# Kernel optimization log

Hardware: AMD Instinct MI355X
Metric: run time of the kernel (lower is better)

Reference implementation:

```python
import jax, jax.numpy as jnp
import numpy as np

CUTOFF = 5.0

def cubic_cutoff(d):
    # f(0)=1, f(y)=0, smooth first derivatives at both ends
    y = CUTOFF
    xc = 1.0 - 1.5 * (d * d) / (y * y) + 0.5 * (d * d * d) / (y * y * y)
    return jnp.where(d <= 0.0, 1.0, jnp.where(d >= y, 0.0, xc))


def setup_inputs() -> dict:
    key = jax.random.key(0)
    ks = jax.random.split(key, 16)
    B, N, H = 64, 64, 128
    h = jax.random.normal(ks[0], (B, N, H), jnp.float32)
    x = jax.random.uniform(ks[1], (B, N, 3), jnp.float32) * 10.0  # 10A box -> partial neighbor sparsity
    node_mask = jnp.ones((B, N), dtype=bool)
    h0 = jax.random.normal(ks[2], (B, N, H), jnp.float32)
    s = lambda fin: 1.0 / np.sqrt(fin)
    # edge_mlp: Linear(2H+1 -> H), SiLU, Linear(H -> H), SiLU
    We1 = jax.random.normal(ks[3], (2 * H + 1, H), jnp.float32) * s(2 * H + 1)
    be1 = jnp.zeros((H,), jnp.float32)
    We2 = jax.random.normal(ks[4], (H, H), jnp.float32) * s(H)
    be2 = jnp.zeros((H,), jnp.float32)
    # node_mlp: Linear(H + residual_nf + H = 3H -> H), SiLU, Linear(H -> H)
    Wn1 = jax.random.normal(ks[5], (3 * H, H), jnp.float32) * s(3 * H)
    bn1 = jnp.zeros((H,), jnp.float32)
    Wn2 = jax.random.normal(ks[6], (H, H), jnp.float32) * s(H)
    bn2 = jnp.zeros((H,), jnp.float32)
    # coord_mlp: Linear(H -> H), SiLU, Linear(H -> 1, no bias, xavier gain=0.001)
    Wc1 = jax.random.normal(ks[7], (H, H), jnp.float32) * s(H)
    bc1 = jnp.zeros((H,), jnp.float32)
    Wc2 = jax.random.normal(ks[8], (H, 1), jnp.float32) * (0.001 * s(H))
    return {"h": h, "x": x, "node_mask": node_mask, "h0": h0,
            "We1": We1, "be1": be1, "We2": We2, "be2": be2,
            "Wn1": Wn1, "bn1": bn1, "Wn2": Wn2, "bn2": bn2,
            "Wc1": Wc1, "bc1": bc1, "Wc2": Wc2}


def reference(h, x, node_mask, h0, We1, be1, We2, be2, Wn1, bn1, Wn2, bn2, Wc1, bc1, Wc2):
    B, N, H = h.shape
    # pairwise distances; distances are detached in the torch default path
    diff = x[:, :, None, :] - x[:, None, :, :]                     # [B,N,N,3]
    d = jax.lax.stop_gradient(jnp.sqrt(jnp.sum(diff * diff, -1)))  # [B,N,N]
    eye = jnp.eye(N, dtype=bool)[None]
    mask = (node_mask[:, :, None] & node_mask[:, None, :]
            & (d < CUTOFF) & (~eye))                               # [B,N,N]
    maskf = mask.astype(h.dtype)
    # edge model: feat[b,j,k] = [h[b,j], h[b,k], d^2]
    feat = jnp.concatenate([
        jnp.broadcast_to(h[:, :, None, :], (B, N, N, H)),
        jnp.broadcast_to(h[:, None, :, :], (B, N, N, H)),
        (d * d)[..., None]], axis=-1)                              # [B,N,N,2H+1]
    e = jax.nn.silu(feat @ We1 + be1)
    e = jax.nn.silu(e @ We2 + be2)
    mij = e * (cubic_cutoff(d) * maskf)[..., None]                 # [B,N,N,H]
    # node model: sum messages into receiver j
    mi = jnp.sum(mij, axis=2)                                      # [B,N,H]
    nfeat = jnp.concatenate([h, mi, h0], axis=-1)                  # [B,N,3H]
    h_out = jax.nn.silu(nfeat @ Wn1 + bn1) @ Wn2 + bn2
    h_new = h + h_out                                              # recurrent
    # coord model (scatter-add semantics of the intended math)
    phi = jax.nn.silu(mij @ Wc1 + bc1) @ Wc2                       # [B,N,N,1]
    C = 1.0 / (N - 1.0)
    x_up = C * jnp.sum(diff * phi * maskf[..., None], axis=2)      # [B,N,3]
    x_new = jnp.clip(x + x_up, -1000.0, 1000.0)
    return (h_new, x_new)
```

## Files before the change

### kernel.cpp

```cpp
#include <hip/hip_runtime.h>

#define Hh 128
#define Nn 64
#define CAP 2048
#define TPB 16

typedef _Float16 f16x8 __attribute__((ext_vector_type(8)));
typedef float f32x4 __attribute__((ext_vector_type(4)));
typedef unsigned int u32;

__device__ __forceinline__ float silu_f(float v){
    return v * __builtin_amdgcn_rcpf(1.0f + __expf(-v));
}
__device__ __forceinline__ int swz(int row, int cb){ return row*256 + (cb ^ ((row & 7) << 4)); }

#define WT_BYTES (9*32768)

__global__ __launch_bounds__(128) void k_w(
    const float* __restrict__ We1, const float* __restrict__ We2, const float* __restrict__ Wc1,
    const float* __restrict__ Wn1, const float* __restrict__ Wn2, char* __restrict__ wT)
{
    if (blockIdx.x == 128){
        if (threadIdx.x < 16){
            f16x8 v;
            #pragma unroll
            for (int i=0;i<8;i++) v[i] = (_Float16)We1[256*Hh + threadIdx.x*8 + i];
            *(f16x8*)(wT + 8*32768 + threadIdx.x*16) = v;
        }
        return;
    }
    const int id  = blockIdx.x*128 + threadIdx.x;
    const int mat = id >> 11;
    const int r   = id & 2047;
    const int n   = r >> 4;
    const int kg  = r & 15;
    const float* __restrict__ src;
    int koff = 0;
    switch (mat){
        case 0: src = We2; break;
        case 1: src = Wc1; break;
        case 2: src = Wn1; break;
        case 3: src = Wn1; koff = 128; break;
        case 4: src = Wn1; koff = 256; break;
        case 5: src = Wn2; break;
        case 6: src = We1; break;
        default: src = We1; koff = 128; break;
    }
    f16x8 v;
    #pragma unroll
    for (int i=0;i<8;i++) v[i] = (_Float16)src[(koff + kg*8 + i)*Hh + n];
    *(f16x8*)(wT + mat*32768 + n*256 + kg*16) = v;
}

__global__ __launch_bounds__(256, 2) void k_preG(
    const float* __restrict__ h, const char* __restrict__ wT, const float* __restrict__ be1,
    _Float16* __restrict__ Aout, _Float16* __restrict__ Bout)
{
    __shared__ __align__(16) char sA[4096];

    const int r0  = blockIdx.x * 16;
    const int tid = threadIdx.x;
    const int w   = tid >> 6;
    const int l   = tid & 63;
    const int lrow= l & 15;
    const int lk  = l >> 4;
    const int n0 = 2*w, n1 = n0 + 1;
    const int colA = n0*16 + lrow, colB = n1*16 + lrow;

    {
        const int row = tid >> 4;
        const int g   = tid & 15;
        const float4* src = (const float4*)(h + (r0+row)*Hh + g*8);
        const float4 v0 = src[0], v1 = src[1];
        f16x8 e;
        e[0]=(_Float16)v0.x; e[1]=(_Float16)v0.y; e[2]=(_Float16)v0.z; e[3]=(_Float16)v0.w;
        e[4]=(_Float16)v1.x; e[5]=(_Float16)v1.y; e[6]=(_Float16)v1.z; e[7]=(_Float16)v1.w;
        *(f16x8*)(sA + swz(row, g*16)) = e;
    }
    __syncthreads();

    const char* WaT = wT + 6*32768;
    const char* WbT = wT + 7*32768;

    f32x4 accA[2], accB[2];
    {
        const float ba = be1[colA], bb = be1[colB];
        accA[0] = (f32x4){ba,ba,ba,ba};
        accA[1] = (f32x4){bb,bb,bb,bb};
        accB[0] = (f32x4){0.f,0.f,0.f,0.f};
        accB[1] = (f32x4){0.f,0.f,0.f,0.f};
    }
    #pragma unroll
    for (int kb=0;kb<4;kb++){
        const int cb = kb*64 + lk*16;
        const f16x8 a   = *(const f16x8*)(sA  + swz(lrow, cb));
        const f16x8 bA0 = *(const f16x8*)(WaT + (n0*16+lrow)*256 + cb);
        const f16x8 bA1 = *(const f16x8*)(WaT + (n1*16+lrow)*256 + cb);
        const f16x8 bB0 = *(const f16x8*)(WbT + (n0*16+lrow)*256 + cb);
        const f16x8 bB1 = *(const f16x8*)(WbT + (n1*16+lrow)*256 + cb);
        accA[0] = __builtin_amdgcn_mfma_f32_16x16x32_f16(a, bA0, accA[0], 0, 0, 0);
        accA[1] = __builtin_amdgcn_mfma_f32_16x16x32_f16(a, bA1, accA[1], 0, 0, 0);
        accB[0] = __builtin_amdgcn_mfma_f32_16x16x32_f16(a, bB0, accB[0], 0, 0, 0);
        accB[1] = __builtin_amdgcn_mfma_f32_16x16x32_f16(a, bB1, accB[1], 0, 0, 0);
    }
    #pragma unroll
    for (int r=0;r<4;r++){
        const int row = r0 + lk*4 + r;
        Aout[row*Hh + colA] = (_Float16)accA[0][r];
        Aout[row*Hh + colB] = (_Float16)accA[1][r];
        Bout[row*Hh + colA] = (_Float16)accB[0][r];
        Bout[row*Hh + colB] = (_Float16)accB[1][r];
    }
}

__global__ __launch_bounds__(256) void k_prep(
    const float* __restrict__ x,
    u32* __restrict__ cntB, u32* __restrict__ off_g, u32* __restrict__ cnt_g,
    u32* __restrict__ code_g, float* __restrict__ d2_g, float* __restrict__ cut_g)
{
    __shared__ float sX[192];
    __shared__ int sCnt[64], sOff[64];
    const int b   = blockIdx.x;
    const int tid = threadIdx.x;
    const int wd  = tid >> 6;
    const int l   = tid & 63;

    if (tid < 192) sX[tid] = x[b*192 + tid];
    __syncthreads();

    for (int jj = 0; jj < 16; jj++){
        const int j = wd*16 + jj;
        const float dx0 = sX[j*3+0]-sX[l*3+0];
        const float dx1 = sX[j*3+1]-sX[l*3+1];
        const float dx2 = sX[j*3+2]-sX[l*3+2];
        const float d2 = dx0*dx0 + dx1*dx1 + dx2*dx2;
        const bool valid = (l != j) && (d2 < 25.0f);
        const unsigned long long bal = __ballot(valid);
        if (l == 0) sCnt[j] = (int)__popcll(bal);
    }
    __syncthreads();
    if (tid < 64){
        int v = sCnt[tid];
        int incl = v;
        #pragma unroll
        for (int off=1; off<64; off<<=1){
            int o = __shfl_up(incl, off);
            if (l >= off) incl += o;
        }
        sOff[tid] = incl - v;
    }
    __syncthreads();
    if (tid < 64){
        off_g[b*64 + tid] = (u32)sOff[tid];
        cnt_g[b*64 + tid] = (u32)sCnt[tid];
        if (tid == 63){
            int tot = sOff[63] + sCnt[63];
            cntB[b] = (u32)(tot > CAP ? CAP : tot);
        }
    }
    for (int jj = 0; jj < 16; jj++){
        const int j = wd*16 + jj;
        const float dx0 = sX[j*3+0]-sX[l*3+0];
        const float dx1 = sX[j*3+1]-sX[l*3+1];
        const float dx2 = sX[j*3+2]-sX[l*3+2];
        const float d2 = dx0*dx0 + dx1*dx1 + dx2*dx2;
        const bool valid = (l != j) && (d2 < 25.0f);
        const unsigned long long bal = __ballot(valid);
        const int pos = __popcll(bal & ((1ull << l) - 1ull));
        if (valid){
            const int dst = sOff[j] + pos;
            if (dst < CAP){
                const int e = b*CAP + dst;
                code_g[e] = (u32)((j << 6) | l);
                d2_g[e]   = d2;
                cut_g[e]  = 1.0f - 0.06f*d2 + 0.004f*d2*sqrtf(d2);
            }
        }
    }
}

__global__ __launch_bounds__(256, 2) void k_edge(
    const _Float16* __restrict__ Ain, const _Float16* __restrict__ Bin,
    const char* __restrict__ wT,
    const float* __restrict__ be2_g, const float* __restrict__ bc1_g, const float* __restrict__ Wc2,
    const u32* __restrict__ cntB, const u32* __restrict__ code_g,
    const float* __restrict__ d2_g, const float* __restrict__ cut_g,
    float* __restrict__ mi_p, float* __restrict__ phi_g)
{
    __shared__ __align__(16) char sEM[32768];
    __shared__ int   sBj[128];
    __shared__ u32   sCode[128];
    __shared__ float sD2[128], sCut[128];
    __shared__ float sPhP[4][128];

    const int bid = blockIdx.x;
    const int b   = bid & 63;
    const int t   = bid >> 6;
    const int E_b = (int)cntB[b];
    const int r0  = t*128;
    if (r0 >= E_b) return;
    const int R   = (E_b - r0 < 128) ? (E_b - r0) : 128;
    const int MT  = (R + 15) >> 4;

    const int tid = threadIdx.x;
    const int w   = tid >> 6;
    const int l   = tid & 63;
    const int lrow= l & 15;
    const int lk  = l >> 4;
    const int n0 = 2*w, n1 = n0 + 1;
    const int colA = n0*16 + lrow, colB = n1*16 + lrow;
    const char* We2T = wT;
    const char* Wc1T = wT + 32768;

    if (tid < 128){
        if (tid < R){
            const u32 c = code_g[b*CAP + r0 + tid];
            sCode[tid] = c;
            sBj[tid]   = (int)(c >> 6);
            sD2[tid]   = d2_g[b*CAP + r0 + tid];
            sCut[tid]  = cut_g[b*CAP + r0 + tid];
        } else {
            sCode[tid] = 0; sBj[tid] = -1; sD2[tid] = 0.f; sCut[tid] = 0.f;
        }
    }
    __syncthreads();

    {
        const f16x8* W6 = (const f16x8*)(wT + 8*32768);
        #pragma unroll
        for (int pass=0; pass<2; pass++){
            const int row = pass*64 + (tid >> 2);
            if (row < MT*16){
                const int q = tid & 3;
                const u32 c = sCode[row];
                const int jl = (int)(c >> 6), kl = (int)(c & 63);
                const _Float16 d2h = (_Float16)sD2[row];
                f16x8 dsplat;
                #pragma unroll
                for (int i=0;i<8;i++) dsplat[i] = d2h;
                const f16x8* Aj = (const f16x8*)(Ain + (b*Nn+jl)*Hh + q*32);
                const f16x8* Bk = (const f16x8*)(Bin + (b*Nn+kl)*Hh + q*32);
                #pragma unroll
                for (int s=0;s<4;s++){
                    f16x8 pre = Aj[s] + Bk[s] + W6[q*4+s]*dsplat;
                    f16x8 e;
                    #pragma unroll
                    for (int i=0;i<8;i++) e[i] = (_Float16)silu_f((float)pre[i]);
                    *(f16x8*)(sEM + swz(row, q*64 + s*16)) = e;
                }
            }
        }
    }
    __syncthreads();

    f32x4 acc[4][2];
    for (int tb = 0; tb < MT; tb += 4){
        const int MTp = (MT - tb < 4) ? (MT - tb) : 4;
        {
            const float b2a = be2_g[colA], b2b = be2_g[colB];
            #pragma unroll
            for (int mt=0;mt<4;mt++){
                acc[mt][0] = (f32x4){b2a,b2a,b2a,b2a};
                acc[mt][1] = (f32x4){b2b,b2b,b2b,b2b};
            }
        }
        #pragma unroll
        for (int kb=0;kb<4;kb++){
            const int cb = kb*64 + lk*16;
            const f16x8 bA = *(const f16x8*)(We2T + (n0*16+lrow)*256 + cb);
            const f16x8 bB = *(const f16x8*)(We2T + (n1*16+lrow)*256 + cb);
            #pragma unroll
            for (int mt=0;mt<4;mt++){
                if (mt < MTp){
                    const f16x8 a = *(const f16x8*)(sEM + swz((tb+mt)*16 + lrow, cb));
                    acc[mt][0] = __builtin_amdgcn_mfma_f32_16x16x32_f16(a, bA, acc[mt][0], 0, 0, 0);
                    acc[mt][1] = __builtin_amdgcn_mfma_f32_16x16x32_f16(a, bB, acc[mt][1], 0, 0, 0);
                }
            }
        }
        #pragma unroll
        for (int mt=0;mt<4;mt++){
            if (mt < MTp){
                #pragma unroll
                for (int r=0;r<4;r++){
                    const int row = (tb+mt)*16 + lk*4 + r;
                    const float m0 = silu_f(acc[mt][0][r]) * sCut[row];
                    const float m1 = silu_f(acc[mt][1][r]) * sCut[row];
                    acc[mt][0][r] = m0; acc[mt][1][r] = m1;
                }
            }
        }
        __syncthreads();
        #pragma unroll
        for (int mt=0;mt<4;mt++){
            if (mt < MTp){
                #pragma unroll
                for (int r=0;r<4;r++){
                    const int row = (tb+mt)*16 + lk*4 + r;
                    const int xr  = (row & 7) << 4;
                    *(_Float16*)(sEM + row*256 + ((colA*2) ^ xr)) = (_Float16)acc[mt][0][r];
                    *(_Float16*)(sEM + row*256 + ((colB*2) ^ xr)) = (_Float16)acc[mt][1][r];
                }
            }
        }
    }
    __syncthreads();

    {
        const int col  = tid & 127;
        const int half = tid >> 7;
        const int slot = (t & 1)*2 + half;
        float sum = 0.f;
        int cur = -1;
        const int rbeg = half*64, rend = rbeg + 64;
        for (int r = rbeg; r < rend; ++r){
            const int bj = sBj[r];
            const float m = (float)(*(const _Float16*)(sEM + r*256 + ((col*2) ^ ((r&7)<<4))));
            if (bj != cur){
                if (cur >= 0) mi_p[((size_t)slot*4096 + (b<<6) + cur)*128 + col] = sum;
                cur = bj; sum = 0.f;
            }
            sum += m;
        }
        if (cur >= 0) mi_p[((size_t)slot*4096 + (b<<6) + cur)*128 + col] = sum;
    }

    for (int tb = 0; tb < MT; tb += 4){
        const int MTp = (MT - tb < 4) ? (MT - tb) : 4;
        {
            const float c1a = bc1_g[colA], c1b = bc1_g[colB];
            #pragma unroll
            for (int mt=0;mt<4;mt++){
                acc[mt][0] = (f32x4){c1a,c1a,c1a,c1a};
                acc[mt][1] = (f32x4){c1b,c1b,c1b,c1b};
            }
        }
        #pragma unroll
        for (int kb=0;kb<4;kb++){
            const int cb = kb*64 + lk*16;
            const f16x8 bA = *(const f16x8*)(Wc1T + (n0*16+lrow)*256 + cb);
            const f16x8 bB = *(const f16x8*)(Wc1T + (n1*16+lrow)*256 + cb);
            #pragma unroll
            for (int mt=0;mt<4;mt++){
                if (mt < MTp){
                    const f16x8 a = *(const f16x8*)(sEM + swz((tb+mt)*16 + lrow, cb));
                    acc[mt][0] = __builtin_amdgcn_mfma_f32_16x16x32_f16(a, bA, acc[mt][0], 0, 0, 0);
                    acc[mt][1] = __builtin_amdgcn_mfma_f32_16x16x32_f16(a, bB, acc[mt][1], 0, 0, 0);
                }
            }
        }
        const float wca = Wc2[colA], wcb = Wc2[colB];
        float php[16];
        #pragma unroll
        for (int mt=0;mt<4;mt++){
            if (mt < MTp){
                #pragma unroll
                for (int r=0;r<4;r++)
                    php[mt*4+r] = silu_f(acc[mt][0][r])*wca + silu_f(acc[mt][1][r])*wcb;
            }
        }
        #pragma unroll
        for (int i=0;i<16;i++){
            if ((i>>2) < MTp){
                php[i] += __shfl_xor(php[i], 1);
                php[i] += __shfl_xor(php[i], 2);
                php[i] += __shfl_xor(php[i], 4);
                php[i] += __shfl_xor(php[i], 8);
            }
        }
        if (lrow == 0){
            #pragma unroll
            for (int mt=0;mt<4;mt++){
                if (mt < MTp){
                    #pragma unroll
                    for (int r=0;r<4;r++)
                        sPhP[w][(tb+mt)*16 + lk*4 + r] = php[mt*4+r];
                }
            }
        }
    }
    __syncthreads();

    if (tid < 128 && tid < R){
        const float phi = sPhP[0][tid] + sPhP[1][tid] + sPhP[2][tid] + sPhP[3][tid];
        phi_g[b*CAP + r0 + tid] = phi;
    }
}

__global__ __launch_bounds__(256) void k_reduce(
    const float* __restrict__ x,
    const u32* __restrict__ off_g, const u32* __restrict__ cnt_g,
    const u32* __restrict__ code_g, const float* __restrict__ phi_g,
    const float* __restrict__ mi_p,
    _Float16* __restrict__ mi_g, float* __restrict__ out_x)
{
    const int tid = threadIdx.x;
    const int wd  = tid >> 6;
    const int l   = tid & 63;
    const int gid = blockIdx.x*4 + wd;
    const int b   = gid >> 6;

    #pragma unroll
    for (int p=0;p<2;p++){
        const int col = l*2 + p;
        const size_t base = (size_t)gid*128 + col;
        const float s = mi_p[base] + mi_p[(size_t)4096*128 + base]
                      + mi_p[(size_t)2*4096*128 + base] + mi_p[(size_t)3*4096*128 + base];
        mi_g[gid*Hh + col] = (_Float16)s;
    }

    const int cnt = (int)cnt_g[gid];
    const int off = (int)off_g[gid];
    float v0=0.f, v1=0.f, v2=0.f;
    if (l < cnt && (off + l) < CAP){
        const int e = b*CAP + off + l;
        const int kl = (int)(code_g[e] & 63);
        const float phi = phi_g[e];
        v0 = (x[gid*3+0] - x[(b*Nn+kl)*3+0]) * phi;
        v1 = (x[gid*3+1] - x[(b*Nn+kl)*3+1]) * phi;
        v2 = (x[gid*3+2] - x[(b*Nn+kl)*3+2]) * phi;
    }
    #pragma unroll
    for (int off2=1; off2<64; off2<<=1){
        v0 += __shfl_xor(v0, off2);
        v1 += __shfl_xor(v1, off2);
        v2 += __shfl_xor(v2, off2);
    }
    if (l == 0){
        const float C = 1.0f/63.0f;
        out_x[gid*3+0] = fminf(fmaxf(x[gid*3+0] + C*v0, -1000.f), 1000.f);
        out_x[gid*3+1] = fminf(fmaxf(x[gid*3+1] + C*v1, -1000.f), 1000.f);
        out_x[gid*3+2] = fminf(fmaxf(x[gid*3+2] + C*v2, -1000.f), 1000.f);
    }
}

__global__ __launch_bounds__(256, 2) void k_node(
    const float* __restrict__ h, const _Float16* __restrict__ mi_g,
    const float* __restrict__ h0,
    const char* __restrict__ wT,
    const float* __restrict__ bn1_g, const float* __restrict__ bn2_g,
    float* __restrict__ out_h)
{
    __shared__ __align__(16) char sA[8192];
    __shared__ __align__(16) char sHid[8192];

    const int r0  = blockIdx.x * 32;
    const int tid = threadIdx.x;
    const int w   = tid >> 6;
    const int l   = tid & 63;
    const int lrow= l & 15;
    const int lk  = l >> 4;
    const int n0 = 2*w, n1 = n0 + 1;
    const int colA = n0*16 + lrow, colB = n1*16 + lrow;

    f32x4 acc[2][2];
    {
        const float b1a = bn1_g[colA], b1b = bn1_g[colB];
        acc[0][0] = (f32x4){b1a,b1a,b1a,b1a};
        acc[0][1] = (f32x4){b1b,b1b,b1b,b1b};
        acc[1][0] = (f32x4){b1a,b1a,b1a,b1a};
        acc[1][1] = (f32x4){b1b,b1b,b1b,b1b};
    }

    const int arow = tid >> 3;
    const int g    = tid & 7;

    for (int c = 0; c < 3; c++){
        if (c == 1){
            const f16x8* src = (const f16x8*)(mi_g + (r0+arow)*Hh + g*16);
            *(f16x8*)(sA + swz(arow, g*32))      = src[0];
            *(f16x8*)(sA + swz(arow, g*32+16))   = src[1];
        } else {
            const float* base = (c == 0) ? h : h0;
            const float4* src = (const float4*)(base + (r0+arow)*Hh + g*16);
            const float4 v0=src[0], v1=src[1], v2=src[2], v3=src[3];
            f16x8 e0, e1;
            e0[0]=(_Float16)v0.x; e0[1]=(_Float16)v0.y; e0[2]=(_Float16)v0.z; e0[3]=(_Float16)v0.w;
            e0[4]=(_Float16)v1.x; e0[5]=(_Float16)v1.y; e0[6]=(_Float16)v1.z; e0[7]=(_Float16)v1.w;
            e1[0]=(_Float16)v2.x; e1[1]=(_Float16)v2.y; e1[2]=(_Float16)v2.z; e1[3]=(_Float16)v2.w;
            e1[4]=(_Float16)v3.x; e1[5]=(_Float16)v3.y; e1[6]=(_Float16)v3.z; e1[7]=(_Float16)v3.w;
            *(f16x8*)(sA + swz(arow, g*32))    = e0;
            *(f16x8*)(sA + swz(arow, g*32+16)) = e1;
        }
        __syncthreads();
        const char* Wimg = wT + (2+c)*32768;
        #pragma unroll
        for (int kb=0;kb<4;kb++){
            const int cb = kb*64 + lk*16;
            const f16x8 bA = *(const f16x8*)(Wimg + (n0*16+lrow)*256 + cb);
            const f16x8 bB = *(const f16x8*)(Wimg + (n1*16+lrow)*256 + cb);
            #pragma unroll
            for (int mt=0;mt<2;mt++){
                const f16x8 a = *(const f16x8*)(sA + swz(mt*16 + lrow, cb));
                acc[mt][0] = __builtin_amdgcn_mfma_f32_16x16x32_f16(a, bA, acc[mt][0], 0, 0, 0);
                acc[mt][1] = __builtin_amdgcn_mfma_f32_16x16x32_f16(a, bB, acc[mt][1], 0, 0, 0);
            }
        }
        __syncthreads();
    }

    #pragma unroll
    for (int mt=0;mt<2;mt++){
        #pragma unroll
        for (int r=0;r<4;r++){
            const int row = mt*16 + lk*4 + r;
            const int xr  = (row & 7) << 4;
            *(_Float16*)(sHid + row*256 + ((colA*2) ^ xr)) = (_Float16)silu_f(acc[mt][0][r]);
            *(_Float16*)(sHid + row*256 + ((colB*2) ^ xr)) = (_Float16)silu_f(acc[mt][1][r]);
        }
    }
    __syncthreads();

    const char* Wn2T = wT + 5*32768;
    f32x4 acc2[2][2];
    {
        const float b2a = bn2_g[colA], b2b = bn2_g[colB];
        acc2[0][0] = (f32x4){b2a,b2a,b2a,b2a};
        acc2[0][1] = (f32x4){b2b,b2b,b2b,b2b};
        acc2[1][0] = (f32x4){b2a,b2a,b2a,b2a};
        acc2[1][1] = (f32x4){b2b,b2b,b2b,b2b};
    }
    #pragma unroll
    for (int kb=0;kb<4;kb++){
        const int cb = kb*64 + lk*16;
        const f16x8 bA = *(const f16x8*)(Wn2T + (n0*16+lrow)*256 + cb);
        const f16x8 bB = *(const f16x8*)(Wn2T + (n1*16+lrow)*256 + cb);
        #pragma unroll
        for (int mt=0;mt<2;mt++){
            const f16x8 a = *(const f16x8*)(sHid + swz(mt*16 + lrow, cb));
            acc2[mt][0] = __builtin_amdgcn_mfma_f32_16x16x32_f16(a, bA, acc2[mt][0], 0, 0, 0);
            acc2[mt][1] = __builtin_amdgcn_mfma_f32_16x16x32_f16(a, bB, acc2[mt][1], 0, 0, 0);
        }
    }
    #pragma unroll
    for (int mt=0;mt<2;mt++){
        #pragma unroll
        for (int r=0;r<4;r++){
            const int row = r0 + mt*16 + lk*4 + r;
            out_h[row*Hh + colA] = h[row*Hh + colA] + acc2[mt][0][r];
            out_h[row*Hh + colB] = h[row*Hh + colB] + acc2[mt][1][r];
        }
    }
}

extern "C" void kernel_launch(void* const* d_in, const int* in_sizes, int n_in,
                              void* d_out, int out_size, void* d_ws, size_t ws_size,
                              hipStream_t stream) {
    const float* h   = (const float*)d_in[0];
    const float* x   = (const float*)d_in[1];
    const float* h0  = (const float*)d_in[3];
    const float* We1 = (const float*)d_in[4];
    const float* be1 = (const float*)d_in[5];
    const float* We2 = (const float*)d_in[6];
    const float* be2 = (const float*)d_in[7];
    const float* Wn1 = (const float*)d_in[8];
    const float* bn1 = (const float*)d_in[9];
    const float* Wn2 = (const float*)d_in[10];
    const float* bn2 = (const float*)d_in[11];
    const float* Wc1 = (const float*)d_in[12];
    const float* bc1 = (const float*)d_in[13];
    const float* Wc2 = (const float*)d_in[14];

    float* out_h = (float*)d_out;
    float* out_x = out_h + 64*64*128;

    char*      wT   = (char*)d_ws;
    _Float16*  A    = (_Float16*)(wT + WT_BYTES);
    _Float16*  Bv   = A + 4096*128;
    _Float16*  mi   = Bv + 4096*128;
    u32*       cntB = (u32*)(mi + 4096*128);
    u32*       offg = cntB + 64;
    u32*       cntg = offg + 4096;
    u32*       code = cntg + 4096;
    float*     d2g  = (float*)(code + 64*CAP);
    float*     cutg = d2g + 64*CAP;
    float*     phig = cutg + 64*CAP;
    float*     mip  = phig + 64*CAP;

    hipMemsetAsync(mip, 0, (size_t)4*4096*128*sizeof(float), stream);
    k_w     <<<129, 128, 0, stream>>>(We1, We2, Wc1, Wn1, Wn2, wT);
    k_preG  <<<256, 256, 0, stream>>>(h, wT, be1, A, Bv);
    k_prep  <<<64, 256, 0, stream>>>(x, cntB, offg, cntg, code, d2g, cutg);
    k_edge  <<<64*TPB, 256, 0, stream>>>(A, Bv, wT, be2, bc1, Wc2,
                                         cntB, code, d2g, cutg, mip, phig);
    k_reduce<<<1024, 256, 0, stream>>>(x, offg, cntg, code, phig, mip, mi, out_x);
    k_node  <<<128, 256, 0, stream>>>(h, mi, h0, wT, bn1, bn2, out_h);
}
```

Before: 93.04 us.

## Fuse weight prep with neighbor prep, split edge LDS, drop partial-sum memset

Merges the weight-transpose kernel and the neighbor-list prep kernel into one launch, with blocks 0-63 building the edge lists and the rest converting weights. The edge kernel now keeps the first hidden layer and the masked messages in separate LDS buffers, so the coord MLP runs before the message segment-sum and one barrier goes away. The memset of the partial message buffer is removed, and the reduce kernel works out from offsets which partial slots each node wrote and reads only those. This cuts a launch, a memset and some global reads, but doubles the edge kernel's LDS to 64KB, which may lower occupancy.

```diff
diff --git a/kernel.cpp b/kernel.cpp
--- a/kernel.cpp
+++ b/kernel.cpp
@@ -16,114 +16,53 @@
 
 #define WT_BYTES (9*32768)
 
-__global__ __launch_bounds__(128) void k_w(
+__global__ __launch_bounds__(256) void k_wp(
+    const float* __restrict__ x,
     const float* __restrict__ We1, const float* __restrict__ We2, const float* __restrict__ Wc1,
-    const float* __restrict__ Wn1, const float* __restrict__ Wn2, char* __restrict__ wT)
-{
-    if (blockIdx.x == 128){
-        if (threadIdx.x < 16){
-            f16x8 v;
-            #pragma unroll
-            for (int i=0;i<8;i++) v[i] = (_Float16)We1[256*Hh + threadIdx.x*8 + i];
-            *(f16x8*)(wT + 8*32768 + threadIdx.x*16) = v;
-        }
-        return;
-    }
-    const int id  = blockIdx.x*128 + threadIdx.x;
-    const int mat = id >> 11;
-    const int r   = id & 2047;
-    const int n   = r >> 4;
-    const int kg  = r & 15;
-    const float* __restrict__ src;
-    int koff = 0;
-    switch (mat){
-        case 0: src = We2; break;
-        case 1: src = Wc1; break;
-        case 2: src = Wn1; break;
-        case 3: src = Wn1; koff = 128; break;
-        case 4: src = Wn1; koff = 256; break;
-        case 5: src = Wn2; break;
-        case 6: src = We1; break;
-        default: src = We1; koff = 128; break;
-    }
-    f16x8 v;
-    #pragma unroll
-    for (int i=0;i<8;i++) v[i] = (_Float16)src[(koff + kg*8 + i)*Hh + n];
-    *(f16x8*)(wT + mat*32768 + n*256 + kg*16) = v;
-}
-
-__global__ __launch_bounds__(256, 2) void k_preG(
-    const float* __restrict__ h, const char* __restrict__ wT, const float* __restrict__ be1,
-    _Float16* __restrict__ Aout, _Float16* __restrict__ Bout)
-{
-    __shared__ __align__(16) char sA[4096];
-
-    const int r0  = blockIdx.x * 16;
-    const int tid = threadIdx.x;
-    const int w   = tid >> 6;
-    const int l   = tid & 63;
-    const int lrow= l & 15;
-    const int lk  = l >> 4;
-    const int n0 = 2*w, n1 = n0 + 1;
-    const int colA = n0*16 + lrow, colB = n1*16 + lrow;
-
-    {
-        const int row = tid >> 4;
-        const int g   = tid & 15;
-        const float4* src = (const float4*)(h + (r0+row)*Hh + g*8);
-        const float4 v0 = src[0], v1 = src[1];
-        f16x8 e;
-        e[0]=(_Float16)v0.x; e[1]=(_Float16)v0.y; e[2]=(_Float16)v0.z; e[3]=(_Float16)v0.w;
-        e[4]=(_Float16)v1.x; e[5]=(_Float16)v1.y; e[6]=(_Float16)v1.z; e[7]=(_Float16)v1.w;
-        *(f16x8*)(sA + swz(row, g*16)) = e;
-    }
-    __syncthreads();
-
-    const char* WaT = wT + 6*32768;
-    const char* WbT = wT + 7*32768;
-
-    f32x4 accA[2], accB[2];
-    {
-        const float ba = be1[colA], bb = be1[colB];
-        accA[0] = (f32x4){ba,ba,ba,ba};
-        accA[1] = (f32x4){bb,bb,bb,bb};
-        accB[0] = (f32x4){0.f,0.f,0.f,0.f};
-        accB[1] = (f32x4){0.f,0.f,0.f,0.f};
-    }
-    #pragma unroll
-    for (int kb=0;kb<4;kb++){
-        const int cb = kb*64 + lk*16;
-        const f16x8 a   = *(const f16x8*)(sA  + swz(lrow, cb));
-        const f16x8 bA0 = *(const f16x8*)(WaT + (n0*16+lrow)*256 + cb);
-        const f16x8 bA1 = *(const f16x8*)(WaT + (n1*16+lrow)*256 + cb);
-        const f16x8 bB0 = *(const f16x8*)(WbT + (n0*16+lrow)*256 + cb);
-        const f16x8 bB1 = *(const f16x8*)(WbT + (n1*16+lrow)*256 + cb);
-        accA[0] = __builtin_amdgcn_mfma_f32_16x16x32_f16(a, bA0, accA[0], 0, 0, 0);
-        accA[1] = __builtin_amdgcn_mfma_f32_16x16x32_f16(a, bA1, accA[1], 0, 0, 0);
-        accB[0] = __builtin_amdgcn_mfma_f32_16x16x32_f16(a, bB0, accB[0], 0, 0, 0);
-        accB[1] = __builtin_amdgcn_mfma_f32_16x16x32_f16(a, bB1, accB[1], 0, 0, 0);
-    }
-    #pragma unroll
-    for (int r=0;r<4;r++){
-        const int row = r0 + lk*4 + r;
-        Aout[row*Hh + colA] = (_Float16)accA[0][r];
-        Aout[row*Hh + colB] = (_Float16)accA[1][r];
-        Bout[row*Hh + colA] = (_Float16)accB[0][r];
-        Bout[row*Hh + colB] = (_Float16)accB[1][r];
-    }
-}
-
-__global__ __launch_bounds__(256) void k_prep(
-    const float* __restrict__ x,
+    const float* __restrict__ Wn1, const float* __restrict__ Wn2, char* __restrict__ wT,
     u32* __restrict__ cntB, u32* __restrict__ off_g, u32* __restrict__ cnt_g,
     u32* __restrict__ code_g, float* __restrict__ d2_g, float* __restrict__ cut_g)
 {
+    const int tid = threadIdx.x;
+    if (blockIdx.x >= 64){
+        if (blockIdx.x == 128){
+            if (tid < 16){
+                f16x8 v;
+                #pragma unroll
+                for (int i=0;i<8;i++) v[i] = (_Float16)We1[256*Hh + tid*8 + i];
+                *(f16x8*)(wT + 8*32768 + tid*16) = v;
+            }
+            return;
+        }
+        const int id  = (blockIdx.x-64)*256 + tid;
+        const int mat = id >> 11;
+        const int r   = id & 2047;
+        const int n   = r >> 4;
+        const int kg  = r & 15;
+        const float* __restrict__ src;
+        int koff = 0;
+        switch (mat){
+            case 0: src = We2; break;
+            case 1: src = Wc1; break;
+            case 2: src = Wn1; break;
+            case 3: src = Wn1; koff = 128; break;
+            case 4: src = Wn1; koff = 256; break;
+            case 5: src = Wn2; break;
+            case 6: src = We1; break;
+            default: src = We1; koff = 128; break;
+        }
+        f16x8 v;
+        #pragma unroll
+        for (int i=0;i<8;i++) v[i] = (_Float16)src[(koff + kg*8 + i)*Hh + n];
+        *(f16x8*)(wT + mat*32768 + n*256 + kg*16) = v;
+        return;
+    }
+
     __shared__ float sX[192];
     __shared__ int sCnt[64], sOff[64];
-    const int b   = blockIdx.x;
-    const int tid = threadIdx.x;
-    const int wd  = tid >> 6;
-    const int l   = tid & 63;
+    const int b  = blockIdx.x;
+    const int wd = tid >> 6;
+    const int l  = tid & 63;
 
     if (tid < 192) sX[tid] = x[b*192 + tid];
     __syncthreads();
@@ -179,6 +118,67 @@
     }
 }
 
+__global__ __launch_bounds__(256, 2) void k_preG(
+    const float* __restrict__ h, const char* __restrict__ wT, const float* __restrict__ be1,
+    _Float16* __restrict__ Aout, _Float16* __restrict__ Bout)
+{
+    __shared__ __align__(16) char sA[4096];
+
+    const int r0  = blockIdx.x * 16;
+    const int tid = threadIdx.x;
+    const int w   = tid >> 6;
+    const int l   = tid & 63;
+    const int lrow= l & 15;
+    const int lk  = l >> 4;
+    const int n0 = 2*w, n1 = n0 + 1;
+    const int colA = n0*16 + lrow, colB = n1*16 + lrow;
+
+    {
+        const int row = tid >> 4;
+        const int g   = tid & 15;
+        const float4* src = (const float4*)(h + (r0+row)*Hh + g*8);
+        const float4 v0 = src[0], v1 = src[1];
+        f16x8 e;
+        e[0]=(_Float16)v0.x; e[1]=(_Float16)v0.y; e[2]=(_Float16)v0.z; e[3]=(_Float16)v0.w;
+        e[4]=(_Float16)v1.x; e[5]=(_Float16)v1.y; e[6]=(_Float16)v1.z; e[7]=(_Float16)v1.w;
+        *(f16x8*)(sA + swz(row, g*16)) = e;
+    }
+    __syncthreads();
+
+    const char* WaT = wT + 6*32768;
+    const char* WbT = wT + 7*32768;
+
+    f32x4 accA[2], accB[2];
+    {
+        const float ba = be1[colA], bb = be1[colB];
+        accA[0] = (f32x4){ba,ba,ba,ba};
+        accA[1] = (f32x4){bb,bb,bb,bb};
+        accB[0] = (f32x4){0.f,0.f,0.f,0.f};
+        accB[1] = (f32x4){0.f,0.f,0.f,0.f};
+    }
+    #pragma unroll
+    for (int kb=0;kb<4;kb++){
+        const int cb = kb*64 + lk*16;
+        const f16x8 a   = *(const f16x8*)(sA  + swz(lrow, cb));
+        const f16x8 bA0 = *(const f16x8*)(WaT + (n0*16+lrow)*256 + cb);
+        const f16x8 bA1 = *(const f16x8*)(WaT + (n1*16+lrow)*256 + cb);
+        const f16x8 bB0 = *(const f16x8*)(WbT + (n0*16+lrow)*256 + cb);
+        const f16x8 bB1 = *(const f16x8*)(WbT + (n1*16+lrow)*256 + cb);
+        accA[0] = __builtin_amdgcn_mfma_f32_16x16x32_f16(a, bA0, accA[0], 0, 0, 0);
+        accA[1] = __builtin_amdgcn_mfma_f32_16x16x32_f16(a, bA1, accA[1], 0, 0, 0);
+        accB[0] = __builtin_amdgcn_mfma_f32_16x16x32_f16(a, bB0, accB[0], 0, 0, 0);
+        accB[1] = __builtin_amdgcn_mfma_f32_16x16x32_f16(a, bB1, accB[1], 0, 0, 0);
+    }
+    #pragma unroll
+    for (int r=0;r<4;r++){
+        const int row = r0 + lk*4 + r;
+        Aout[row*Hh + colA] = (_Float16)accA[0][r];
+        Aout[row*Hh + colB] = (_Float16)accA[1][r];
+        Bout[row*Hh + colA] = (_Float16)accB[0][r];
+        Bout[row*Hh + colB] = (_Float16)accB[1][r];
+    }
+}
+
 __global__ __launch_bounds__(256, 2) void k_edge(
     const _Float16* __restrict__ Ain, const _Float16* __restrict__ Bin,
     const char* __restrict__ wT,
@@ -187,7 +187,8 @@
     const float* __restrict__ d2_g, const float* __restrict__ cut_g,
     float* __restrict__ mi_p, float* __restrict__ phi_g)
 {
-    __shared__ __align__(16) char sEM[32768];
+    __shared__ __align__(16) char sE1[32768];
+    __shared__ __align__(16) char sM[32768];
     __shared__ int   sBj[128];
     __shared__ u32   sCode[128];
     __shared__ float sD2[128], sCut[128];
@@ -246,7 +247,7 @@
                     f16x8 e;
                     #pragma unroll
                     for (int i=0;i<8;i++) e[i] = (_Float16)silu_f((float)pre[i]);
-                    *(f16x8*)(sEM + swz(row, q*64 + s*16)) = e;
+                    *(f16x8*)(sE1 + swz(row, q*64 + s*16)) = e;
                 }
             }
         }
@@ -272,7 +273,7 @@
             #pragma unroll
             for (int mt=0;mt<4;mt++){
                 if (mt < MTp){
-                    const f16x8 a = *(const f16x8*)(sEM + swz((tb+mt)*16 + lrow, cb));
+                    const f16x8 a = *(const f16x8*)(sE1 + swz((tb+mt)*16 + lrow, cb));
                     acc[mt][0] = __builtin_amdgcn_mfma_f32_16x16x32_f16(a, bA, acc[mt][0], 0, 0, 0);
                     acc[mt][1] = __builtin_amdgcn_mfma_f32_16x16x32_f16(a, bB, acc[mt][1], 0, 0, 0);
                 }
@@ -286,25 +287,69 @@
                     const int row = (tb+mt)*16 + lk*4 + r;
                     const float m0 = silu_f(acc[mt][0][r]) * sCut[row];
                     const float m1 = silu_f(acc[mt][1][r]) * sCut[row];
-                    acc[mt][0][r] = m0; acc[mt][1][r] = m1;
+                    const int xr  = (row & 7) << 4;
+                    *(_Float16*)(sM + row*256 + ((colA*2) ^ xr)) = (_Float16)m0;
+                    *(_Float16*)(sM + row*256 + ((colB*2) ^ xr)) = (_Float16)m1;
                 }
             }
         }
-        __syncthreads();
+    }
+    __syncthreads();
+
+    for (int tb = 0; tb < MT; tb += 4){
+        const int MTp = (MT - tb < 4) ? (MT - tb) : 4;
+        {
+            const float c1a = bc1_g[colA], c1b = bc1_g[colB];
+            #pragma unroll
+            for (int mt=0;mt<4;mt++){
+                acc[mt][0] = (f32x4){c1a,c1a,c1a,c1a};
+                acc[mt][1] = (f32x4){c1b,c1b,c1b,c1b};
+            }
+        }
+        #pragma unroll
+        for (int kb=0;kb<4;kb++){
+            const int cb = kb*64 + lk*16;
+            const f16x8 bA = *(const f16x8*)(Wc1T + (n0*16+lrow)*256 + cb);
+            const f16x8 bB = *(const f16x8*)(Wc1T + (n1*16+lrow)*256 + cb);
+            #pragma unroll
+            for (int mt=0;mt<4;mt++){
+                if (mt < MTp){
+                    const f16x8 a = *(const f16x8*)(sM + swz((tb+mt)*16 + lrow, cb));
+                    acc[mt][0] = __builtin_amdgcn_mfma_f32_16x16x32_f16(a, bA, acc[mt][0], 0, 0, 0);
+                    acc[mt][1] = __builtin_amdgcn_mfma_f32_16x16x32_f16(a, bB, acc[mt][1], 0, 0, 0);
+                }
+            }
+        }
+        const float wca = Wc2[colA], wcb = Wc2[colB];
+        float php[16];
         #pragma unroll
         for (int mt=0;mt<4;mt++){
             if (mt < MTp){
                 #pragma unroll
-                for (int r=0;r<4;r++){
-                    const int row = (tb+mt)*16 + lk*4 + r;
-                    const int xr  = (row & 7) << 4;
-                    *(_Float16*)(sEM + row*256 + ((colA*2) ^ xr)) = (_Float16)acc[mt][0][r];
-                    *(_Float16*)(sEM + row*256 + ((colB*2) ^ xr)) = (_Float16)acc[mt][1][r];
+                for (int r=0;r<4;r++)
+                    php[mt*4+r] = silu_f(acc[mt][0][r])*wca + silu_f(acc[mt][1][r])*wcb;
+            }
+        }
+        #pragma unroll
+        for (int i=0;i<16;i++){
+            if ((i>>2) < MTp){
+                php[i] += __shfl_xor(php[i], 1);
+                php[i] += __shfl_xor(php[i], 2);
+                php[i] += __shfl_xor(php[i], 4);
+                php[i] += __shfl_xor(php[i], 8);
+            }
+        }
+        if (lrow == 0){
+            #pragma unroll
+            for (int mt=0;mt<4;mt++){
+                if (mt < MTp){
+                    #pragma unroll
+                    for (int r=0;r<4;r++)
+                        sPhP[w][(tb+mt)*16 + lk*4 + r] = php[mt*4+r];
                 }
             }
         }
     }
-    __syncthreads();
 
     {
         const int col  = tid & 127;
@@ -315,7 +360,7 @@
         const int rbeg = half*64, rend = rbeg + 64;
         for (int r = rbeg; r < rend; ++r){
             const int bj = sBj[r];
-            const float m = (float)(*(const _Float16*)(sEM + r*256 + ((col*2) ^ ((r&7)<<4))));
+            const float m = (float)(*(const _Float16*)(sM + r*256 + ((col*2) ^ ((r&7)<<4))));
             if (bj != cur){
                 if (cur >= 0) mi_p[((size_t)slot*4096 + (b<<6) + cur)*128 + col] = sum;
                 cur = bj; sum = 0.f;
@@ -323,61 +368,6 @@
             sum += m;
         }
         if (cur >= 0) mi_p[((size_t)slot*4096 + (b<<6) + cur)*128 + col] = sum;
-    }
-
-    for (int tb = 0; tb < MT; tb += 4){
-        const int MTp = (MT - tb < 4) ? (MT - tb) : 4;
-        {
-            const float c1a = bc1_g[colA], c1b = bc1_g[colB];
-            #pragma unroll
-            for (int mt=0;mt<4;mt++){
-                acc[mt][0] = (f32x4){c1a,c1a,c1a,c1a};
-                acc[mt][1] = (f32x4){c1b,c1b,c1b,c1b};
-            }
-        }
-        #pragma unroll
-        for (int kb=0;kb<4;kb++){
-            const int cb = kb*64 + lk*16;
-            const f16x8 bA = *(const f16x8*)(Wc1T + (n0*16+lrow)*256 + cb);
-            const f16x8 bB = *(const f16x8*)(Wc1T + (n1*16+lrow)*256 + cb);
-            #pragma unroll
-            for (int mt=0;mt<4;mt++){
-                if (mt < MTp){
-                    const f16x8 a = *(const f16x8*)(sEM + swz((tb+mt)*16 + lrow, cb));
-                    acc[mt][0] = __builtin_amdgcn_mfma_f32_16x16x32_f16(a, bA, acc[mt][0], 0, 0, 0);
-                    acc[mt][1] = __builtin_amdgcn_mfma_f32_16x16x32_f16(a, bB, acc[mt][1], 0, 0, 0);
-                }
-            }
-        }
-        const float wca = Wc2[colA], wcb = Wc2[colB];
-        float php[16];
-        #pragma unroll
-        for (int mt=0;mt<4;mt++){
-            if (mt < MTp){
-                #pragma unroll
-                for (int r=0;r<4;r++)
-                    php[mt*4+r] = silu_f(acc[mt][0][r])*wca + silu_f(acc[mt][1][r])*wcb;
-            }
-        }
-        #pragma unroll
-        for (int i=0;i<16;i++){
-            if ((i>>2) < MTp){
-                php[i] += __shfl_xor(php[i], 1);
-                php[i] += __shfl_xor(php[i], 2);
-                php[i] += __shfl_xor(php[i], 4);
-                php[i] += __shfl_xor(php[i], 8);
-            }
-        }
-        if (lrow == 0){
-            #pragma unroll
-            for (int mt=0;mt<4;mt++){
-                if (mt < MTp){
-                    #pragma unroll
-                    for (int r=0;r<4;r++)
-                        sPhP[w][(tb+mt)*16 + lk*4 + r] = php[mt*4+r];
-                }
-            }
-        }
     }
     __syncthreads();
 
@@ -400,37 +390,58 @@
     const int gid = blockIdx.x*4 + wd;
     const int b   = gid >> 6;
 
+    const int cnt = (int)cnt_g[gid];
+    const int off = (int)off_g[gid];
+
+    bool v0=false, v1=false, v2=false, v3=false;
+    if (cnt > 0){
+        const int t0 = off >> 7;
+        const int t1 = (off + cnt - 1) >> 7;
+        {
+            const int s0 = off - t0*128;
+            const int e0 = ((off+cnt) < (t0+1)*128 ? (off+cnt) : (t0+1)*128) - t0*128;
+            const bool h0 = (s0 < 64), h1 = (e0 > 64);
+            if ((t0 & 1) == 0){ v0 |= h0; v1 |= h1; } else { v2 |= h0; v3 |= h1; }
+        }
+        if (t1 != t0){
+            const int e0 = (off + cnt) - t1*128;
+            const bool h0 = true, h1 = (e0 > 64);
+            if ((t1 & 1) == 0){ v0 |= h0; v1 |= h1; } else { v2 |= h0; v3 |= h1; }
+        }
+    }
+
     #pragma unroll
     for (int p=0;p<2;p++){
         const int col = l*2 + p;
         const size_t base = (size_t)gid*128 + col;
-        const float s = mi_p[base] + mi_p[(size_t)4096*128 + base]
-                      + mi_p[(size_t)2*4096*128 + base] + mi_p[(size_t)3*4096*128 + base];
+        float s = 0.f;
+        if (v0) s += mi_p[base];
+        if (v1) s += mi_p[(size_t)4096*128 + base];
+        if (v2) s += mi_p[(size_t)2*4096*128 + base];
+        if (v3) s += mi_p[(size_t)3*4096*128 + base];
         mi_g[gid*Hh + col] = (_Float16)s;
     }
 
-    const int cnt = (int)cnt_g[gid];
-    const int off = (int)off_g[gid];
-    float v0=0.f, v1=0.f, v2=0.f;
+    float w0=0.f, w1=0.f, w2=0.f;
     if (l < cnt && (off + l) < CAP){
         const int e = b*CAP + off + l;
         const int kl = (int)(code_g[e] & 63);
         const float phi = phi_g[e];
-        v0 = (x[gid*3+0] - x[(b*Nn+kl)*3+0]) * phi;
-        v1 = (x[gid*3+1] - x[(b*Nn+kl)*3+1]) * phi;
-        v2 = (x[gid*3+2] - x[(b*Nn+kl)*3+2]) * phi;
+        w0 = (x[gid*3+0] - x[(b*Nn+kl)*3+0]) * phi;
+        w1 = (x[gid*3+1] - x[(b*Nn+kl)*3+1]) * phi;
+        w2 = (x[gid*3+2] - x[(b*Nn+kl)*3+2]) * phi;
     }
     #pragma unroll
     for (int off2=1; off2<64; off2<<=1){
-        v0 += __shfl_xor(v0, off2);
-        v1 += __shfl_xor(v1, off2);
-        v2 += __shfl_xor(v2, off2);
+        w0 += __shfl_xor(w0, off2);
+        w1 += __shfl_xor(w1, off2);
+        w2 += __shfl_xor(w2, off2);
     }
     if (l == 0){
         const float C = 1.0f/63.0f;
-        out_x[gid*3+0] = fminf(fmaxf(x[gid*3+0] + C*v0, -1000.f), 1000.f);
-        out_x[gid*3+1] = fminf(fmaxf(x[gid*3+1] + C*v1, -1000.f), 1000.f);
-        out_x[gid*3+2] = fminf(fmaxf(x[gid*3+2] + C*v2, -1000.f), 1000.f);
+        out_x[gid*3+0] = fminf(fmaxf(x[gid*3+0] + C*w0, -1000.f), 1000.f);
+        out_x[gid*3+1] = fminf(fmaxf(x[gid*3+1] + C*w1, -1000.f), 1000.f);
+        out_x[gid*3+2] = fminf(fmaxf(x[gid*3+2] + C*w2, -1000.f), 1000.f);
     }
 }
 
@@ -577,10 +588,9 @@
     float*     phig = cutg + 64*CAP;
     float*     mip  = phig + 64*CAP;
 
-    hipMemsetAsync(mip, 0, (size_t)4*4096*128*sizeof(float), stream);
-    k_w     <<<129, 128, 0, stream>>>(We1, We2, Wc1, Wn1, Wn2, wT);
+    k_wp    <<<129, 256, 0, stream>>>(x, We1, We2, Wc1, Wn1, Wn2, wT,
+                                      cntB, offg, cntg, code, d2g, cutg);
     k_preG  <<<256, 256, 0, stream>>>(h, wT, be1, A, Bv);
-    k_prep  <<<64, 256, 0, stream>>>(x, cntB, offg, cntg, code, d2g, cutg);
     k_edge  <<<64*TPB, 256, 0, stream>>>(A, Bv, wT, be2, bc1, Wc2,
                                          cntB, code, d2g, cutg, mip, phig);
     k_reduce<<<1024, 256, 0, stream>>>(x, offg, cntg, code, phig, mip, mi, out_x);
```

Result: faster. 83.57 us (-10.2%).
